# Optimization experiments

Hardware: AMD Instinct MI355X
Metric: run time of the kernel (lower is better)

Reference implementation:

```python
import jax, jax.numpy as jnp
import numpy as np

B, N, NPOINT = 8, 32768, 2048
C_FEAT = 67  # 3 + 64
INIT_DIST = 1e10


def furthest_point_sample(pts, npoint):
    """Iterative FPS. pts: (B, N, C). Returns int32 idx (B, npoint).
    Matches pointnet2 kernel: idx[0]=0, temp init to 1e10, temp=min(temp, d2(last)),
    next = argmax(temp)."""
    b, n, _ = pts.shape

    def step(carry, _):
        temp, last_idx = carry
        last = jnp.take_along_axis(pts, last_idx[:, None, None], axis=1)  # (B,1,C)
        d2 = jnp.sum((pts - last) ** 2, axis=-1)  # (B,N)
        temp = jnp.minimum(temp, d2)
        nxt = jnp.argmax(temp, axis=1).astype(jnp.int32)
        return (temp, nxt), last_idx

    temp0 = jnp.full((b, n), INIT_DIST, dtype=pts.dtype)
    idx0 = jnp.zeros((b,), dtype=jnp.int32)
    _, idxs = jax.lax.scan(step, (temp0, idx0), None, length=npoint)
    return jnp.transpose(idxs)  # (B, npoint)


def gather_points(x_t, idx):
    """x_t: (B, C, N), idx: (B, npoint) -> (B, C, npoint)."""
    return jnp.take_along_axis(x_t, idx[:, None, :].astype(jnp.int32), axis=2)


def setup_inputs() -> dict:
    key = jax.random.key(0)
    k1, k2 = jax.random.split(key)
    points_xyz = jax.random.normal(k1, (B, N, 3), dtype=jnp.float32) * 30.0
    points_xyz_t = jnp.transpose(points_xyz, (0, 2, 1))  # (B,3,N)
    features_with_xyz = jax.random.normal(k2, (B, C_FEAT, N), dtype=jnp.float32)
    return {"points_xyz": points_xyz, "points_xyz_t": points_xyz_t,
            "features_with_xyz": features_with_xyz}


def reference(points_xyz, points_xyz_t, features_with_xyz):
    # Points_Sampler with num_point=[2048], fps_mod_list=['D-FPS'],
    # fps_sample_range_list=[-1]: single D-FPS over the whole range.
    idx = furthest_point_sample(points_xyz, NPOINT)          # (B, npoint)
    out = gather_points(points_xyz_t, idx)                   # (B, 3, npoint)
    return out
```

## Files before the change

kernel.cpp:

```cpp
#include <hip/hip_runtime.h>

#define BATCH 8
#define KSPLIT 8
#define NBLK (BATCH * KSPLIT)
#define N 32768
#define NPOINT 2048
#define NT 256
#define QB (N / 2 / KSPLIT)

typedef __attribute__((ext_vector_type(2))) float f2;


#define REP8(M)  M(0) M(1) M(2) M(3) M(4) M(5) M(6) M(7)
#define REP8R(M) M(7) M(6) M(5) M(4) M(3) M(2) M(1) M(0)

#define DPP_UMAX(v, ctrl) {                                                  \
    unsigned _t = (unsigned)__builtin_amdgcn_update_dpp(                     \
        0, (int)(v), (ctrl), 0xf, 0xf, true);                                \
    (v) = (v) > _t ? (v) : _t; }

__device__ __forceinline__ unsigned wave_umax(unsigned v) {
    DPP_UMAX(v, 0x111);
    DPP_UMAX(v, 0x112);
    DPP_UMAX(v, 0x114);
    DPP_UMAX(v, 0x118);
    DPP_UMAX(v, 0x142);
    DPP_UMAX(v, 0x143);
    return (unsigned)__builtin_amdgcn_readlane((int)v, 63);
}

#define QP_U64MAX(v, ctrl) {                                                 \
    unsigned _lo = (unsigned)__builtin_amdgcn_update_dpp(                    \
        0, (int)(unsigned)(v), (ctrl), 0xf, 0xf, false);                     \
    unsigned _hi = (unsigned)__builtin_amdgcn_update_dpp(                    \
        0, (int)(unsigned)((v) >> 32), (ctrl), 0xf, 0xf, false);             \
    unsigned long long _p = ((unsigned long long)_hi << 32) | _lo;           \
    (v) = _p > (v) ? _p : (v); }

__device__ __forceinline__ unsigned long long rdlane_u64(unsigned long long v,
                                                         int lane) {
    const unsigned lo = (unsigned)__builtin_amdgcn_readlane(
        (int)(unsigned)v, lane);
    const unsigned hi = (unsigned)__builtin_amdgcn_readlane(
        (int)(unsigned)(v >> 32), lane);
    return ((unsigned long long)hi << 32) | lo;
}

__global__ __attribute__((amdgpu_flat_work_group_size(NT, NT),
                          amdgpu_waves_per_eu(2, 2)))
void fps_kernel(const float* __restrict__ pts_t,
                float* __restrict__ out,
                unsigned long long* __restrict__ gslot)
{
#pragma clang fp contract(off)
    __shared__ unsigned long long s_key[NPOINT];
    __shared__ unsigned long long s_res[2];

    const int blk = blockIdx.x;
    const int b = blk & (BATCH - 1);
    const int k = blk >> 3;
    const int t = threadIdx.x;
    const int w = t >> 6;
    const int l = t & 63;

    const float* __restrict__ px = pts_t + (size_t)b * 3 * N;
    const float* __restrict__ py = px + N;
    const float* __restrict__ pz = py + N;
    const f2* __restrict__ px2 = (const f2*)px;
    const f2* __restrict__ py2 = (const f2*)py;
    const f2* __restrict__ pz2 = (const f2*)pz;
    float* outx = out + (size_t)b * 3 * NPOINT;
    float* outy = outx + NPOINT;
    float* outz = outy + NPOINT;

    unsigned long long* __restrict__ slotb =
        gslot + (size_t)b * NPOINT * KSPLIT;

#define DECL(g) f2 x##g, y##g, z##g, T##g;
    REP8(DECL)
#undef DECL

#define LOADG(g) { const int q = k * QB + (g) * NT + t;           \
                   x##g = px2[q]; y##g = py2[q]; z##g = pz2[q];   \
                   T##g = (f2){1e10f, 1e10f}; }
    REP8(LOADG)
#undef LOADG

    for (int i = t; i < NPOINT; i += NT) s_key[i] = 0ull;

    float lx = px[0], ly = py[0], lz = pz[0];
    if (k == 0 && t == 0) { outx[0] = lx; outy[0] = ly; outz[0] = lz; }
    __syncthreads();

    for (int j = 1; j < NPOINT; ++j) {
        const f2 lx2 = (f2){lx, lx};
        const f2 ly2 = (f2){ly, ly};
        const f2 lz2 = (f2){lz, lz};

        f2 mx = (f2){0.0f, 0.0f};
#define UPD(g) { f2 dz = z##g - lz2;                                     \
                 f2 dx = x##g - lx2;                                     \
                 f2 dy = y##g - ly2;                                     \
                 f2 s  = (dx * dx + dy * dy) + dz * dz; \
                 T##g.x = fminf(T##g.x, s.x);                            \
                 T##g.y = fminf(T##g.y, s.y);                            \
                 mx.x = fmaxf(mx.x, T##g.x);                             \
                 mx.y = fmaxf(mx.y, T##g.y); }
        REP8(UPD)
#undef UPD
        const float vlane = fmaxf(mx.x, mx.y);

        int cand = N;
#define SCANG(g) { const int q = k * QB + (g) * NT + t;           \
                   cand = (T##g.y == vlane) ? 2 * q + 1 : cand;   \
                   cand = (T##g.x == vlane) ? 2 * q     : cand; }
        REP8R(SCANG)
#undef SCANG

        const unsigned vbits = __float_as_uint(vlane);
        const unsigned Mbits = wave_umax(vbits);
        const unsigned uidx  = wave_umax(vbits == Mbits ? (unsigned)(N - cand)
                                                        : 0u);
        const unsigned long long key =
            ((unsigned long long)Mbits << 32) | uidx;

        if (l == 0) atomicMax(&s_key[j], key);
        __syncthreads();

        unsigned long long* __restrict__ slots = slotb + (size_t)j * KSPLIT;
        if (w == 0) {
            if (l == 0)
                __hip_atomic_store(&slots[k], s_key[j], __ATOMIC_RELAXED,
                                   __HIP_MEMORY_SCOPE_AGENT);
            unsigned long long o = 0ull;
            if (l < KSPLIT) {
                do {
                    o = __hip_atomic_load(&slots[l], __ATOMIC_RELAXED,
                                          __HIP_MEMORY_SCOPE_AGENT);
                } while (o == 0ull);
            }
            QP_U64MAX(o, 0xB1);
            QP_U64MAX(o, 0x4E);
            const unsigned long long m03 = rdlane_u64(o, 0);
            const unsigned long long m47 = rdlane_u64(o, 4);
            const unsigned long long K = m47 > m03 ? m47 : m03;
            if (l == 0) s_res[j & 1] = K;
        }
        __syncthreads();

        const unsigned long long K = s_res[j & 1];
        const int sel =
            __builtin_amdgcn_readfirstlane(N - (int)(unsigned)(K & 0xffffffffu));
        lx = px[sel];
        ly = py[sel];
        lz = pz[sel];
        if (k == 0 && t == 0) { outx[j] = lx; outy[j] = ly; outz[j] = lz; }
    }
}

extern "C" void kernel_launch(void* const* d_in, const int* in_sizes, int n_in,
                              void* d_out, int out_size, void* d_ws, size_t ws_size,
                              hipStream_t stream) {
    const float* pts_t = (const float*)d_in[1];
    float* out = (float*)d_out;
    unsigned long long* gslot = (unsigned long long*)d_ws;
    hipMemsetAsync(d_ws, 0,
                   (size_t)BATCH * NPOINT * KSPLIT * sizeof(unsigned long long),
                   stream);
    fps_kernel<<<NBLK, NT, 0, stream>>>(pts_t, out, gslot);
}
```

Measured before the change: 2.723 ms.

## Replace block barriers with per-step LDS flag slots for intra-block reduction

Both __syncthreads per FPS iteration are removed. Waves 1-3 publish their keys to per-iteration LDS slots, and wave 0 spins on them, combines them with its own key, does the cross-block exchange, then publishes the result to a per-iteration LDS slot that the other waves poll. The aim is to cut barrier cost on the 2047-step serial critical path. In exchange, LDS use grows to about 64KB, waves now busy-wait and contend for issue, and correctness depends on relaxed LDS atomics being visible without fences.

```diff
diff --git a/kernel.cpp b/kernel.cpp
--- a/kernel.cpp
+++ b/kernel.cpp
@@ -6,6 +6,7 @@
 #define N 32768
 #define NPOINT 2048
 #define NT 256
+#define NW (NT / 64)
 #define QB (N / 2 / KSPLIT)
 
 typedef __attribute__((ext_vector_type(2))) float f2;
@@ -53,8 +54,8 @@
                 unsigned long long* __restrict__ gslot)
 {
 #pragma clang fp contract(off)
-    __shared__ unsigned long long s_key[NPOINT];
-    __shared__ unsigned long long s_res[2];
+    __shared__ unsigned long long s_wkey[NPOINT][3];
+    __shared__ unsigned long long s_res[NPOINT];
 
     const int blk = blockIdx.x;
     const int b = blk & (BATCH - 1);
@@ -86,7 +87,11 @@
     REP8(LOADG)
 #undef LOADG
 
-    for (int i = t; i < NPOINT; i += NT) s_key[i] = 0ull;
+    {
+        unsigned long long* s0 = &s_wkey[0][0];
+        for (int i = t; i < NPOINT * 3; i += NT) s0[i] = 0ull;
+        for (int i = t; i < NPOINT; i += NT) s_res[i] = 0ull;
+    }
 
     float lx = px[0], ly = py[0], lz = pz[0];
     if (k == 0 && t == 0) { outx[0] = lx; outy[0] = ly; outz[0] = lz; }
@@ -124,31 +129,51 @@
         const unsigned long long key =
             ((unsigned long long)Mbits << 32) | uidx;
 
-        if (l == 0) atomicMax(&s_key[j], key);
-        __syncthreads();
-
-        unsigned long long* __restrict__ slots = slotb + (size_t)j * KSPLIT;
-        if (w == 0) {
+        unsigned long long K;
+        if (w > 0) {
             if (l == 0)
-                __hip_atomic_store(&slots[k], s_key[j], __ATOMIC_RELAXED,
-                                   __HIP_MEMORY_SCOPE_AGENT);
-            unsigned long long o = 0ull;
-            if (l < KSPLIT) {
+                __hip_atomic_store(&s_wkey[j][w - 1], key, __ATOMIC_RELAXED,
+                                   __HIP_MEMORY_SCOPE_WORKGROUP);
+            do {
+                K = __hip_atomic_load(&s_res[j], __ATOMIC_RELAXED,
+                                      __HIP_MEMORY_SCOPE_WORKGROUP);
+            } while (K == 0ull);
+        } else {
+            unsigned long long o = key;
+            if (l < 3) {
                 do {
-                    o = __hip_atomic_load(&slots[l], __ATOMIC_RELAXED,
-                                          __HIP_MEMORY_SCOPE_AGENT);
+                    o = __hip_atomic_load(&s_wkey[j][l], __ATOMIC_RELAXED,
+                                          __HIP_MEMORY_SCOPE_WORKGROUP);
                 } while (o == 0ull);
             }
             QP_U64MAX(o, 0xB1);
             QP_U64MAX(o, 0x4E);
-            const unsigned long long m03 = rdlane_u64(o, 0);
-            const unsigned long long m47 = rdlane_u64(o, 4);
-            const unsigned long long K = m47 > m03 ? m47 : m03;
-            if (l == 0) s_res[j & 1] = K;
+            const unsigned long long bk = rdlane_u64(o, 0);
+
+            unsigned long long* __restrict__ slots =
+                slotb + (size_t)j * KSPLIT;
+            if (l == 0)
+                __hip_atomic_store(&slots[k], bk, __ATOMIC_RELAXED,
+                                   __HIP_MEMORY_SCOPE_AGENT);
+
+            unsigned long long g = 0ull;
+            if (l < KSPLIT) {
+                do {
+                    g = __hip_atomic_load(&slots[l], __ATOMIC_RELAXED,
+                                          __HIP_MEMORY_SCOPE_AGENT);
+                } while (g == 0ull);
+            }
+            QP_U64MAX(g, 0xB1);
+            QP_U64MAX(g, 0x4E);
+            const unsigned long long m03 = rdlane_u64(g, 0);
+            const unsigned long long m47 = rdlane_u64(g, 4);
+            K = m47 > m03 ? m47 : m03;
+
+            if (l == 0)
+                __hip_atomic_store(&s_res[j], K, __ATOMIC_RELAXED,
+                                   __HIP_MEMORY_SCOPE_WORKGROUP);
         }
-        __syncthreads();
 
-        const unsigned long long K = s_res[j & 1];
         const int sel =
             __builtin_amdgcn_readfirstlane(N - (int)(unsigned)(K & 0xffffffffu));
         lx = px[sel];
```

Measured after the change: 2.705 ms. About the same (-0.7%).
